# Kernel optimization log

Hardware: AMD Instinct MI355X
Metric: run time of the kernel (lower is better)

Reference implementation:

```python
import jax, jax.numpy as jnp
import numpy as np
import math

DIM = 32
M_CONST = 10000.0
TIME_SCALE = 30000.0 / 500.0 * 0.3  # 18.0


def sinusoidal_emb(x):
    # x: [...] -> [..., DIM]
    half = DIM // 2
    freqs = jnp.exp(jnp.arange(half, dtype=x.dtype) * (-math.log(M_CONST) / half))
    ang = x[..., None] * freqs  # [..., half]
    return jnp.concatenate([jnp.sin(ang), jnp.cos(ang)], axis=-1)


def setup_inputs() -> dict:
    key = jax.random.key(0)
    k1, k2, k3, k4 = jax.random.split(key, 4)
    B, N = 2, 1024
    pos = jax.random.normal(k1, (B, N, 3), dtype=jnp.float32)
    time = jax.random.normal(k2, (B, N), dtype=jnp.float32)
    # nn.Linear(32, 32) params
    lim = 1.0 / math.sqrt(DIM)
    W = jax.random.uniform(k3, (DIM, DIM), minval=-lim, maxval=lim, dtype=jnp.float32)
    b = jax.random.uniform(k4, (DIM,), minval=-lim, maxval=lim, dtype=jnp.float32)
    return {"pos": pos, "time": time, "W": W, "b": b}


def reference(pos, time, W, b):
    # pairwise squared spatial distance minus scaled squared time difference
    dpos = pos[:, :, None, :] - pos[:, None, :, :]          # [B,N,N,3]
    dt = (time[:, :, None] - time[:, None, :]) * TIME_SCALE  # [B,N,N]
    ds2 = jnp.sum(dpos * dpos, axis=-1) - dt * dt            # [B,N,N]
    a = jnp.abs(ds2)
    d = jnp.sign(ds2) * jnp.sqrt(a)
    emb = sinusoidal_emb(1024.0 * jnp.clip(d, -4.0, 4.0))    # [B,N,N,DIM]
    rel_attn = jnp.einsum('bnmd,ed->bnme', emb, W) + b       # Linear(dim,dim)
    return (rel_attn, emb)
```

## Files before the change

### kernel.cpp

```cpp
#include <hip/hip_runtime.h>
#include <hip/hip_bf16.h>

typedef __bf16 bf16x8 __attribute__((ext_vector_type(8)));
typedef float  f32x4  __attribute__((ext_vector_type(4)));

__constant__ __device__ const float FREQ8[8] = {
    1.0f, 0.5623413251903491f, 0.31622776601683794f, 0.17782794100389228f,
    0.1f, 0.05623413251903491f, 0.031622776601683794f, 0.017782794100389228f };

template<bool POW2>
__global__ __launch_bounds__(256) void relds_mfma(
    const float* __restrict__ pos,
    const float* __restrict__ tim,
    const float* __restrict__ W,
    const float* __restrict__ bias,
    float* __restrict__ out_attn,
    float* __restrict__ out_emb,
    int N, int NN, int P, int logN)
{
    const int tid  = threadIdx.x;
    const int lane = tid & 63;
    const int wave = tid >> 6;
    const int row  = lane & 15;
    const int kb   = lane >> 4;

    bf16x8 Bf[2];
    float  bv[2];
    #pragma unroll
    for (int n = 0; n < 2; ++n) {
        const int e = n * 16 + row;
        const float4 wA = *reinterpret_cast<const float4*>(W + e * 32 + kb * 8);
        const float4 wB = *reinterpret_cast<const float4*>(W + e * 32 + kb * 8 + 4);
        Bf[n][0] = (__bf16)wA.x; Bf[n][1] = (__bf16)wA.y;
        Bf[n][2] = (__bf16)wA.z; Bf[n][3] = (__bf16)wA.w;
        Bf[n][4] = (__bf16)wB.x; Bf[n][5] = (__bf16)wB.y;
        Bf[n][6] = (__bf16)wB.z; Bf[n][7] = (__bf16)wB.w;
        bv[n] = bias[e];
    }

    const int wbase = blockIdx.x * 256 + wave * 64;
    if (wbase >= P) return;

    constexpr float INV2PI = 0.15915494309189535f;
    const float premul = INV2PI * ((kb & 1) ? 0.01f : 1.0f);
    const float qoff   = (kb >= 2) ? 0.25f : 0.0f;

    f32x4 acc[4][2];
    #pragma unroll
    for (int t = 0; t < 4; ++t)
        #pragma unroll
        for (int n = 0; n < 2; ++n)
            #pragma unroll
            for (int r = 0; r < 4; ++r) acc[t][n][r] = bv[n];

    #pragma unroll
    for (int t = 0; t < 4; ++t) {
        const int q  = wbase + t * 16 + row;
        const int qc = (q < P) ? q : (P - 1);
        int in_n, in_m;
        if (POW2) {
            in_n = qc >> logN;
            in_m = ((qc >> (2 * logN)) << logN) | (qc & (N - 1));
        } else {
            const int b_ = qc / NN; const int r_ = qc - b_ * NN;
            const int n_ = r_ / N;  const int m_ = r_ - n_ * N;
            in_n = b_ * N + n_;     in_m = b_ * N + m_;
        }
        const float dx = pos[in_n * 3 + 0] - pos[in_m * 3 + 0];
        const float dy = pos[in_n * 3 + 1] - pos[in_m * 3 + 1];
        const float dz = pos[in_n * 3 + 2] - pos[in_m * 3 + 2];
        const float dt = (tim[in_n] - tim[in_m]) * 18.0f;
        const float ds2 = dx * dx + dy * dy + dz * dz - dt * dt;
        const float d   = copysignf(sqrtf(fabsf(ds2)), ds2);
        const float x   = 1024.0f * fminf(4.0f, fmaxf(-4.0f, d));
        const float xr  = x * premul;

        float v[8];
        #pragma unroll
        for (int j = 0; j < 8; ++j) {
            float rr = fmaf(xr, FREQ8[j], qoff);
            rr -= floorf(rr);
            v[j] = __builtin_amdgcn_sinf(rr);
        }

        if (q < P) {
            float* ep = out_emb + (size_t)q * 32 + kb * 8;
            reinterpret_cast<float4*>(ep)[0] = make_float4(v[0], v[1], v[2], v[3]);
            reinterpret_cast<float4*>(ep)[1] = make_float4(v[4], v[5], v[6], v[7]);
        }

        bf16x8 Af;
        #pragma unroll
        for (int j = 0; j < 8; ++j) Af[j] = (__bf16)v[j];
        acc[t][0] = __builtin_amdgcn_mfma_f32_16x16x32_bf16(Af, Bf[0], acc[t][0], 0, 0, 0);
        acc[t][1] = __builtin_amdgcn_mfma_f32_16x16x32_bf16(Af, Bf[1], acc[t][1], 0, 0, 0);
    }

    #pragma unroll
    for (int t = 0; t < 4; ++t) {
        const int prow = wbase + t * 16 + kb * 4;
        #pragma unroll
        for (int n = 0; n < 2; ++n) {
            #pragma unroll
            for (int r = 0; r < 4; ++r) {
                if (prow + r < P)
                    out_attn[(size_t)(prow + r) * 32 + n * 16 + row] = acc[t][n][r];
            }
        }
    }
}

extern "C" void kernel_launch(void* const* d_in, const int* in_sizes, int n_in,
                              void* d_out, int out_size, void* d_ws, size_t ws_size,
                              hipStream_t stream) {
    const float* pos  = (const float*)d_in[0];
    const float* tim  = (const float*)d_in[1];
    const float* W    = (const float*)d_in[2];
    const float* bias = (const float*)d_in[3];

    const int BN = in_sizes[1];
    const int P  = out_size / 64;
    const int N  = P / BN;
    const int NN = N * N;

    int logN = 0;
    while ((1 << logN) < N) ++logN;
    const bool pow2 = ((1 << logN) == N);

    float* out_attn = (float*)d_out;
    float* out_emb  = out_attn + (size_t)out_size / 2;

    const int grid = (P + 255) / 256;
    if (pow2)
        relds_mfma<true><<<grid, 256, 0, stream>>>(pos, tim, W, bias, out_attn, out_emb, N, NN, P, logN);
    else
        relds_mfma<false><<<grid, 256, 0, stream>>>(pos, tim, W, bias, out_attn, out_emb, N, NN, P, logN);
}
```

Baseline: 110.8 us.

## Swap MFMA operands to emit vectorized float4 attn stores, use nontemporal stores

The MFMA operands are swapped so the weight tile becomes A and the embedding becomes B. This transposes the accumulator layout, so each lane now holds four consecutive output features of a single pair row. The attn output is therefore written as two 16-byte vector stores per tile instead of eight scalar strided stores. The bias is loaded as a float4 to match the new layout. Both outputs now use nontemporal stores to reduce cache pollution in this write-bound kernel.

```diff
diff --git a/kernel.cpp b/kernel.cpp
--- a/kernel.cpp
+++ b/kernel.cpp
@@ -24,18 +24,19 @@
     const int row  = lane & 15;
     const int kb   = lane >> 4;
 
-    bf16x8 Bf[2];
-    float  bv[2];
+    bf16x8 Wf[2];
+    f32x4  bq[2];
     #pragma unroll
     for (int n = 0; n < 2; ++n) {
         const int e = n * 16 + row;
         const float4 wA = *reinterpret_cast<const float4*>(W + e * 32 + kb * 8);
         const float4 wB = *reinterpret_cast<const float4*>(W + e * 32 + kb * 8 + 4);
-        Bf[n][0] = (__bf16)wA.x; Bf[n][1] = (__bf16)wA.y;
-        Bf[n][2] = (__bf16)wA.z; Bf[n][3] = (__bf16)wA.w;
-        Bf[n][4] = (__bf16)wB.x; Bf[n][5] = (__bf16)wB.y;
-        Bf[n][6] = (__bf16)wB.z; Bf[n][7] = (__bf16)wB.w;
-        bv[n] = bias[e];
+        Wf[n][0] = (__bf16)wA.x; Wf[n][1] = (__bf16)wA.y;
+        Wf[n][2] = (__bf16)wA.z; Wf[n][3] = (__bf16)wA.w;
+        Wf[n][4] = (__bf16)wB.x; Wf[n][5] = (__bf16)wB.y;
+        Wf[n][6] = (__bf16)wB.z; Wf[n][7] = (__bf16)wB.w;
+        const float4 bb = *reinterpret_cast<const float4*>(bias + n * 16 + kb * 4);
+        bq[n][0] = bb.x; bq[n][1] = bb.y; bq[n][2] = bb.z; bq[n][3] = bb.w;
     }
 
     const int wbase = blockIdx.x * 256 + wave * 64;
@@ -49,9 +50,7 @@
     #pragma unroll
     for (int t = 0; t < 4; ++t)
         #pragma unroll
-        for (int n = 0; n < 2; ++n)
-            #pragma unroll
-            for (int r = 0; r < 4; ++r) acc[t][n][r] = bv[n];
+        for (int n = 0; n < 2; ++n) acc[t][n] = bq[n];
 
     #pragma unroll
     for (int t = 0; t < 4; ++t) {
@@ -85,27 +84,26 @@
 
         if (q < P) {
             float* ep = out_emb + (size_t)q * 32 + kb * 8;
-            reinterpret_cast<float4*>(ep)[0] = make_float4(v[0], v[1], v[2], v[3]);
-            reinterpret_cast<float4*>(ep)[1] = make_float4(v[4], v[5], v[6], v[7]);
+            f32x4 e0 = { v[0], v[1], v[2], v[3] };
+            f32x4 e1 = { v[4], v[5], v[6], v[7] };
+            __builtin_nontemporal_store(e0, reinterpret_cast<f32x4*>(ep));
+            __builtin_nontemporal_store(e1, reinterpret_cast<f32x4*>(ep) + 1);
         }
 
         bf16x8 Af;
         #pragma unroll
         for (int j = 0; j < 8; ++j) Af[j] = (__bf16)v[j];
-        acc[t][0] = __builtin_amdgcn_mfma_f32_16x16x32_bf16(Af, Bf[0], acc[t][0], 0, 0, 0);
-        acc[t][1] = __builtin_amdgcn_mfma_f32_16x16x32_bf16(Af, Bf[1], acc[t][1], 0, 0, 0);
+        acc[t][0] = __builtin_amdgcn_mfma_f32_16x16x32_bf16(Wf[0], Af, acc[t][0], 0, 0, 0);
+        acc[t][1] = __builtin_amdgcn_mfma_f32_16x16x32_bf16(Wf[1], Af, acc[t][1], 0, 0, 0);
     }
 
     #pragma unroll
     for (int t = 0; t < 4; ++t) {
-        const int prow = wbase + t * 16 + kb * 4;
-        #pragma unroll
-        for (int n = 0; n < 2; ++n) {
-            #pragma unroll
-            for (int r = 0; r < 4; ++r) {
-                if (prow + r < P)
-                    out_attn[(size_t)(prow + r) * 32 + n * 16 + row] = acc[t][n][r];
-            }
+        const int q = wbase + t * 16 + row;
+        if (q < P) {
+            float* ap = out_attn + (size_t)q * 32 + kb * 4;
+            __builtin_nontemporal_store(acc[t][0], reinterpret_cast<f32x4*>(ap));
+            __builtin_nontemporal_store(acc[t][1], reinterpret_cast<f32x4*>(ap + 16));
         }
     }
 }
```

Result: slower. 203.1 us (+83.4%).
